# Performance work log

Hardware: AMD Instinct MI355X
Metric: run time of the kernel (lower is better)

## Reference

```python
import jax, jax.numpy as jnp
import numpy as np

SHRINK_THRES = 0.0025
EPS = 1e-12  # F.normalize default eps


def _l2norm(v, axis=-1):
    return v / jnp.maximum(jnp.linalg.norm(v, axis=axis, keepdims=True), EPS)


def setup_inputs() -> dict:
    key = jax.random.key(0)
    ks = jax.random.split(key, 5)
    N, C, H, W = 16, 256, 64, 64
    mem_dim = 512
    x = jax.random.normal(ks[0], (N, C, H, W), dtype=jnp.float32)
    memory = jax.random.normal(ks[1], (mem_dim, C), dtype=jnp.float32) * 0.1
    memory = _l2norm(memory, axis=1)
    w1 = jax.random.normal(ks[2], (C, C // 2), dtype=jnp.float32) * (1.0 / np.sqrt(C))
    b1 = jnp.zeros((C // 2,), dtype=jnp.float32)
    w2 = jax.random.normal(ks[3], (C // 2, C), dtype=jnp.float32) * (1.0 / np.sqrt(C // 2))
    b2 = jnp.zeros((C,), dtype=jnp.float32)
    return {"x": x, "memory": memory, "w1": w1, "b1": b1, "w2": w2, "b2": b2}


def reference(x, memory, w1, b1, w2, b2):
    N, C, H, W = x.shape
    # [N,C,H,W] -> [N*H*W, C]
    x_flat = jnp.transpose(x, (0, 2, 3, 1)).reshape(-1, C)
    x_norm = _l2norm(x_flat, axis=1)
    # shared MLP over memory slots: Linear -> ReLU -> Linear -> ReLU
    m = jax.nn.relu(memory @ w1 + b1)
    m = jax.nn.relu(m @ w2 + b2)
    mem_norm = _l2norm(m, axis=1)  # [M, C]
    # cosine similarity + softmax over memory slots
    att = jax.nn.softmax(x_norm @ mem_norm.T, axis=1)  # [N*H*W, M]
    # hard shrink + L1 renormalization
    att = jax.nn.relu(att - SHRINK_THRES)
    att = att / jnp.maximum(jnp.sum(att, axis=1, keepdims=True), EPS)
    out_flat = att @ mem_norm  # [N*H*W, C]
    output = jnp.transpose(out_flat.reshape(N, H, W, C), (0, 3, 1, 2))
    att_map = jnp.transpose(att.reshape(N, H, W, -1), (0, 3, 1, 2))
    return output, att_map
```

## Files before the change

### kernel.cpp

```cpp
#include <hip/hip_runtime.h>
#include <hip/hip_bf16.h>

typedef _Float16 half8 __attribute__((ext_vector_type(8)));
typedef _Float16 half4v __attribute__((ext_vector_type(4)));
typedef float floatx4 __attribute__((ext_vector_type(4)));

#define C_DIM 256
#define M_DIM 512
#define HW 4096
#define TAU 0.0025f
#define LCAP 96

__global__ __launch_bounds__(128) void prep_kernel(
    const float* __restrict__ memory, const float* __restrict__ w1,
    const float* __restrict__ b1, const float* __restrict__ w2,
    const float* __restrict__ b2,
    _Float16* __restrict__ mN, float* __restrict__ mN32,
    float* __restrict__ attmap)
{
  __shared__ float sm[256];
  __shared__ float sh[128];
  __shared__ float s_part[2];
  __shared__ float s_tot;
  const int r = blockIdx.x;
  const int t = threadIdx.x;

  {
    const floatx4 z = {0.f, 0.f, 0.f, 0.f};
    floatx4* p4 = (floatx4*)attmap;
    size_t i = (size_t)r * 128 + t;
#pragma unroll 4
    for (int k = 0; k < 128; ++k) { p4[i] = z; i += 65536; }
  }

  sm[t]       = memory[r * C_DIM + t];
  sm[t + 128] = memory[r * C_DIM + t + 128];
  __syncthreads();
  float acc = b1[t];
#pragma unroll 8
  for (int c = 0; c < 256; ++c) acc = fmaf(sm[c], w1[c * 128 + t], acc);
  sh[t] = fmaxf(acc, 0.f);
  __syncthreads();
  float o0 = b2[t], o1 = b2[t + 128];
#pragma unroll 8
  for (int k = 0; k < 128; ++k) {
    float h = sh[k];
    o0 = fmaf(h, w2[k * 256 + t], o0);
    o1 = fmaf(h, w2[k * 256 + t + 128], o1);
  }
  o0 = fmaxf(o0, 0.f);
  o1 = fmaxf(o1, 0.f);
  float ss = o0 * o0 + o1 * o1;
#pragma unroll
  for (int off = 32; off >= 1; off >>= 1) ss += __shfl_down(ss, off);
  if ((t & 63) == 0) s_part[t >> 6] = ss;
  __syncthreads();
  if (t == 0) s_tot = s_part[0] + s_part[1];
  __syncthreads();
  const float inv = 1.f / fmaxf(sqrtf(s_tot), 1e-12f);
  const float v0 = o0 * inv, v1 = o1 * inv;
  mN[r * C_DIM + t]        = (_Float16)v0;
  mN[r * C_DIM + t + 128]  = (_Float16)v1;
  mN32[r * C_DIM + t]       = v0;
  mN32[r * C_DIM + t + 128] = v1;
}

#define MFMA16(a, b, c) __builtin_amdgcn_mfma_f32_16x16x32_f16(a, b, c, 0, 0, 0)

__global__ __launch_bounds__(512, 4) void main_kernel(
    const float* __restrict__ x,
    const _Float16* __restrict__ mN,
    const float* __restrict__ mN32,
    float* __restrict__ out, float* __restrict__ attmap)
{
  __shared__ _Float16       Xh[64][264];
  __shared__ unsigned short s_lslot[64][LCAP];
  __shared__ float          s_lval[64][LCAP];
  __shared__ int      s_cnt[64];
  __shared__ float    s_sumsq[64];
  __shared__ float    s_sum1[64];
  __shared__ float    s_sum2[64];

  const int tid  = threadIdx.x;
  const int wave = tid >> 6;
  const int lane = tid & 63;
  const int q    = lane >> 4;
  const int c16  = lane & 15;
  const int g    = tid >> 3;
  const int pxq  = tid & 7;

  const int blk = blockIdx.x;
  const int img = blk >> 6;
  const int hw0 = (blk & 63) * 64;
  const float* __restrict__ xb = x + (size_t)img * C_DIM * HW + hw0;

  if (tid < 64) {
    s_sumsq[tid] = 0.f; s_sum1[tid] = 0.f; s_sum2[tid] = 0.f; s_cnt[tid] = 0;
  }
  __syncthreads();

#pragma unroll
  for (int h = 0; h < 2; ++h) {
    floatx4 v[4];
#pragma unroll
    for (int i = 0; i < 4; ++i)
      v[i] = *(const floatx4*)(xb + (size_t)(4 * g + i) * HW + (pxq + 8 * h) * 4);
    float ps[4];
#pragma unroll
    for (int j = 0; j < 4; ++j) {
      const int p = (pxq + 8 * h) * 4 + j;
      half4v hv = {(_Float16)v[0][j], (_Float16)v[1][j], (_Float16)v[2][j], (_Float16)v[3][j]};
      *(half4v*)&Xh[p][4 * g] = hv;
      ps[j] = v[0][j] * v[0][j] + v[1][j] * v[1][j] + v[2][j] * v[2][j] + v[3][j] * v[3][j];
    }
#pragma unroll
    for (int off = 8; off < 64; off <<= 1)
#pragma unroll
      for (int j = 0; j < 4; ++j) ps[j] += __shfl_xor(ps[j], off);
    if ((lane >> 3) == 0) {
#pragma unroll
      for (int j = 0; j < 4; ++j) atomicAdd(&s_sumsq[4 * (lane & 7) + 32 * h + j], ps[j]);
    }
  }

  const _Float16* bp[4];
#pragma unroll
  for (int nt = 0; nt < 4; ++nt)
    bp[nt] = mN + (size_t)(wave * 64 + nt * 16 + c16) * C_DIM + q * 8;
  half8 bcur[4], bnxt[4];
#pragma unroll
  for (int nt = 0; nt < 4; ++nt) bcur[nt] = *(const half8*)bp[nt];

  __syncthreads();

  floatx4 acc[4][4];
#pragma unroll
  for (int mt = 0; mt < 4; ++mt)
#pragma unroll
    for (int nt = 0; nt < 4; ++nt) {
      floatx4 z = {0.f, 0.f, 0.f, 0.f};
      acc[mt][nt] = z;
    }
#pragma unroll
  for (int kb = 0; kb < 8; ++kb) {
    if (kb < 7) {
#pragma unroll
      for (int nt = 0; nt < 4; ++nt) bnxt[nt] = *(const half8*)(bp[nt] + (kb + 1) * 32);
    }
    const int k0 = kb * 32 + q * 8;
    half8 ah[4];
#pragma unroll
    for (int mt = 0; mt < 4; ++mt) ah[mt] = *(const half8*)&Xh[mt * 16 + c16][k0];
#pragma unroll
    for (int nt = 0; nt < 4; ++nt)
#pragma unroll
      for (int mt = 0; mt < 4; ++mt)
        acc[mt][nt] = MFMA16(ah[mt], bcur[nt], acc[mt][nt]);
#pragma unroll
    for (int nt = 0; nt < 4; ++nt) bcur[nt] = bnxt[nt];
  }

#pragma unroll
  for (int mt = 0; mt < 4; ++mt)
#pragma unroll
    for (int r = 0; r < 4; ++r) {
      const int m = mt * 16 + q * 4 + r;
      const float iv = 1.f / fmaxf(sqrtf(s_sumsq[m]), 1e-12f);
      float s = 0.f;
#pragma unroll
      for (int nt = 0; nt < 4; ++nt) {
        const float e = __expf(acc[mt][nt][r] * iv);
        acc[mt][nt][r] = e;
        s += e;
      }
      s += __shfl_xor(s, 1);
      s += __shfl_xor(s, 2);
      s += __shfl_xor(s, 4);
      s += __shfl_xor(s, 8);
      if (c16 == 0) atomicAdd(&s_sum1[m], s);
    }
  __syncthreads();

#pragma unroll
  for (int mt = 0; mt < 4; ++mt)
#pragma unroll
    for (int r = 0; r < 4; ++r) {
      const int m = mt * 16 + q * 4 + r;
      const float isum = 1.f / s_sum1[m];
      float s = 0.f;
#pragma unroll
      for (int nt = 0; nt < 4; ++nt) {
        const float tv = fmaxf(acc[mt][nt][r] * isum - TAU, 0.f);
        acc[mt][nt][r] = tv;
        s += tv;
      }
      s += __shfl_xor(s, 1);
      s += __shfl_xor(s, 2);
      s += __shfl_xor(s, 4);
      s += __shfl_xor(s, 8);
      if (c16 == 0) atomicAdd(&s_sum2[m], s);
    }
  __syncthreads();

#pragma unroll
  for (int mt = 0; mt < 4; ++mt) {
    float rs[4];
#pragma unroll
    for (int r = 0; r < 4; ++r)
      rs[r] = 1.f / fmaxf(s_sum2[mt * 16 + q * 4 + r], 1e-12f);
#pragma unroll
    for (int nt = 0; nt < 4; ++nt) {
      floatx4 a4 = acc[mt][nt];
      const unsigned n = wave * 64 + nt * 16 + c16;
#pragma unroll
      for (int r = 0; r < 4; ++r) {
        a4[r] *= rs[r];
        if (a4[r] > 0.f) {
          const int m = mt * 16 + q * 4 + r;
          const int idx = atomicAdd(&s_cnt[m], 1);
          if (idx < LCAP) {
            s_lslot[m][idx] = (unsigned short)n;
            s_lval[m][idx]  = a4[r];
          }
          attmap[((size_t)img * M_DIM + n) * HW + hw0 + m] = a4[r];
        }
      }
    }
  }
  __syncthreads();

  const int px4 = (tid & 15) * 4;
  const int chg = tid >> 4;
  floatx4 f[8] = {{0.f,0.f,0.f,0.f},{0.f,0.f,0.f,0.f},{0.f,0.f,0.f,0.f},{0.f,0.f,0.f,0.f},
                  {0.f,0.f,0.f,0.f},{0.f,0.f,0.f,0.f},{0.f,0.f,0.f,0.f},{0.f,0.f,0.f,0.f}};
#pragma unroll
  for (int p = 0; p < 4; ++p) {
    const int cn = min(s_cnt[px4 + p], LCAP);
    for (int j = 0; j < cn; ++j) {
      const int slot  = s_lslot[px4 + p][j];
      const float v   = s_lval[px4 + p][j];
      const floatx4* row = (const floatx4*)(mN32 + (size_t)slot * C_DIM + chg * 8);
      const floatx4 r0 = row[0], r1 = row[1];
      f[0][p] += v * r0[0]; f[1][p] += v * r0[1];
      f[2][p] += v * r0[2]; f[3][p] += v * r0[3];
      f[4][p] += v * r1[0]; f[5][p] += v * r1[1];
      f[6][p] += v * r1[2]; f[7][p] += v * r1[3];
    }
  }

#pragma unroll
  for (int c = 0; c < 8; ++c)
    *(floatx4*)(out + ((size_t)img * C_DIM + chg * 8 + c) * HW + hw0 + px4) = f[c];
}

extern "C" void kernel_launch(void* const* d_in, const int* in_sizes, int n_in,
                              void* d_out, int out_size, void* d_ws, size_t ws_size,
                              hipStream_t stream) {
  (void)in_sizes; (void)n_in; (void)out_size; (void)ws_size;
  const float* x      = (const float*)d_in[0];
  const float* memory = (const float*)d_in[1];
  const float* w1     = (const float*)d_in[2];
  const float* b1     = (const float*)d_in[3];
  const float* w2     = (const float*)d_in[4];
  const float* b2     = (const float*)d_in[5];
  float* out    = (float*)d_out;
  float* attmap = out + (size_t)16 * C_DIM * HW;

  _Float16* mN   = (_Float16*)d_ws;
  float*    mN32 = (float*)((char*)d_ws + (size_t)M_DIM * C_DIM * sizeof(_Float16));

  hipLaunchKernelGGL(prep_kernel, dim3(M_DIM), dim3(128), 0, stream,
                     memory, w1, b1, w2, b2, mN, mN32, attmap);
  hipLaunchKernelGGL(main_kernel, dim3(1024), dim3(512), 0, stream,
                     x, mN, mN32, out, attmap);
}
```

Baseline: 323.5 us.

## Halve pixel tile, widen attmap zeroing grid, use nontemporal stores

The main kernel now processes 32 pixels per block instead of 64, doubling the grid to 2048 blocks and raising the occupancy hint to 6. The sparse slot list capacity drops from 96 to 16. The B-operand register double buffering is removed. The prep kernel runs 2048 blocks of 256 threads so the attmap zero-fill is spread wider, and it and the output writes use nontemporal stores. The aim is more parallelism and less LDS per block. LCAP=16 risks silently dropping nonzero attention entries when more than 16 slots survive the shrink threshold.

```diff
diff --git a/kernel.cpp b/kernel.cpp
--- a/kernel.cpp
+++ b/kernel.cpp
@@ -1,5 +1,4 @@
 #include <hip/hip_runtime.h>
-#include <hip/hip_bf16.h>
 
 typedef _Float16 half8 __attribute__((ext_vector_type(8)));
 typedef _Float16 half4v __attribute__((ext_vector_type(4)));
@@ -9,9 +8,9 @@
 #define M_DIM 512
 #define HW 4096
 #define TAU 0.0025f
-#define LCAP 96
-
-__global__ __launch_bounds__(128) void prep_kernel(
+#define LCAP 16
+
+__global__ __launch_bounds__(256) void prep_kernel(
     const float* __restrict__ memory, const float* __restrict__ w1,
     const float* __restrict__ b1, const float* __restrict__ w2,
     const float* __restrict__ b2,
@@ -27,59 +26,69 @@
 
   {
     const floatx4 z = {0.f, 0.f, 0.f, 0.f};
-    floatx4* p4 = (floatx4*)attmap;
-    size_t i = (size_t)r * 128 + t;
-#pragma unroll 4
-    for (int k = 0; k < 128; ++k) { p4[i] = z; i += 65536; }
-  }
-
-  sm[t]       = memory[r * C_DIM + t];
-  sm[t + 128] = memory[r * C_DIM + t + 128];
-  __syncthreads();
-  float acc = b1[t];
+    floatx4* p4 = (floatx4*)attmap + (size_t)r * 4096 + t;
+#pragma unroll
+    for (int k = 0; k < 16; ++k) __builtin_nontemporal_store(z, p4 + k * 256);
+  }
+  if (r >= M_DIM) return;
+
+  if (t < 128) {
+    sm[t]       = memory[r * C_DIM + t];
+    sm[t + 128] = memory[r * C_DIM + t + 128];
+  }
+  __syncthreads();
+  float o0 = 0.f, o1 = 0.f;
+  if (t < 128) {
+    float acc = b1[t];
 #pragma unroll 8
-  for (int c = 0; c < 256; ++c) acc = fmaf(sm[c], w1[c * 128 + t], acc);
-  sh[t] = fmaxf(acc, 0.f);
-  __syncthreads();
-  float o0 = b2[t], o1 = b2[t + 128];
+    for (int c = 0; c < 256; ++c) acc = fmaf(sm[c], w1[c * 128 + t], acc);
+    sh[t] = fmaxf(acc, 0.f);
+  }
+  __syncthreads();
+  if (t < 128) {
+    o0 = b2[t];
+    o1 = b2[t + 128];
 #pragma unroll 8
-  for (int k = 0; k < 128; ++k) {
-    float h = sh[k];
-    o0 = fmaf(h, w2[k * 256 + t], o0);
-    o1 = fmaf(h, w2[k * 256 + t + 128], o1);
-  }
-  o0 = fmaxf(o0, 0.f);
-  o1 = fmaxf(o1, 0.f);
-  float ss = o0 * o0 + o1 * o1;
-#pragma unroll
-  for (int off = 32; off >= 1; off >>= 1) ss += __shfl_down(ss, off);
-  if ((t & 63) == 0) s_part[t >> 6] = ss;
+    for (int k = 0; k < 128; ++k) {
+      float h = sh[k];
+      o0 = fmaf(h, w2[k * 256 + t], o0);
+      o1 = fmaf(h, w2[k * 256 + t + 128], o1);
+    }
+    o0 = fmaxf(o0, 0.f);
+    o1 = fmaxf(o1, 0.f);
+    float ss = o0 * o0 + o1 * o1;
+#pragma unroll
+    for (int off = 32; off >= 1; off >>= 1) ss += __shfl_down(ss, off);
+    if ((t & 63) == 0) s_part[t >> 6] = ss;
+  }
   __syncthreads();
   if (t == 0) s_tot = s_part[0] + s_part[1];
   __syncthreads();
-  const float inv = 1.f / fmaxf(sqrtf(s_tot), 1e-12f);
-  const float v0 = o0 * inv, v1 = o1 * inv;
-  mN[r * C_DIM + t]        = (_Float16)v0;
-  mN[r * C_DIM + t + 128]  = (_Float16)v1;
-  mN32[r * C_DIM + t]       = v0;
-  mN32[r * C_DIM + t + 128] = v1;
+  if (t < 128) {
+    const float inv = 1.f / fmaxf(sqrtf(s_tot), 1e-12f);
+    const float v0 = o0 * inv, v1 = o1 * inv;
+    mN[r * C_DIM + t]        = (_Float16)v0;
+    mN[r * C_DIM + t + 128]  = (_Float16)v1;
+    mN32[r * C_DIM + t]       = v0;
+    mN32[r * C_DIM + t + 128] = v1;
+  }
 }
 
 #define MFMA16(a, b, c) __builtin_amdgcn_mfma_f32_16x16x32_f16(a, b, c, 0, 0, 0)
 
-__global__ __launch_bounds__(512, 4) void main_kernel(
+__global__ __launch_bounds__(512, 6) void main_kernel(
     const float* __restrict__ x,
     const _Float16* __restrict__ mN,
     const float* __restrict__ mN32,
     float* __restrict__ out, float* __restrict__ attmap)
 {
-  __shared__ _Float16       Xh[64][264];
-  __shared__ unsigned short s_lslot[64][LCAP];
-  __shared__ float          s_lval[64][LCAP];
-  __shared__ int      s_cnt[64];
-  __shared__ float    s_sumsq[64];
-  __shared__ float    s_sum1[64];
-  __shared__ float    s_sum2[64];
+  __shared__ _Float16       Xh[32][264];
+  __shared__ unsigned short s_lslot[32][LCAP];
+  __shared__ float          s_lval[32][LCAP];
+  __shared__ int      s_cnt[32];
+  __shared__ float    s_sumsq[32];
+  __shared__ float    s_sum1[32];
+  __shared__ float    s_sum2[32];
 
   const int tid  = threadIdx.x;
   const int wave = tid >> 6;
@@ -90,25 +99,24 @@
   const int pxq  = tid & 7;
 
   const int blk = blockIdx.x;
-  const int img = blk >> 6;
-  const int hw0 = (blk & 63) * 64;
+  const int img = blk >> 7;
+  const int hw0 = (blk & 127) * 32;
   const float* __restrict__ xb = x + (size_t)img * C_DIM * HW + hw0;
 
-  if (tid < 64) {
+  if (tid < 32) {
     s_sumsq[tid] = 0.f; s_sum1[tid] = 0.f; s_sum2[tid] = 0.f; s_cnt[tid] = 0;
   }
   __syncthreads();
 
-#pragma unroll
-  for (int h = 0; h < 2; ++h) {
+  {
     floatx4 v[4];
 #pragma unroll
     for (int i = 0; i < 4; ++i)
-      v[i] = *(const floatx4*)(xb + (size_t)(4 * g + i) * HW + (pxq + 8 * h) * 4);
+      v[i] = *(const floatx4*)(xb + (size_t)(4 * g + i) * HW + pxq * 4);
     float ps[4];
 #pragma unroll
     for (int j = 0; j < 4; ++j) {
-      const int p = (pxq + 8 * h) * 4 + j;
+      const int p = pxq * 4 + j;
       half4v hv = {(_Float16)v[0][j], (_Float16)v[1][j], (_Float16)v[2][j], (_Float16)v[3][j]};
       *(half4v*)&Xh[p][4 * g] = hv;
       ps[j] = v[0][j] * v[0][j] + v[1][j] * v[1][j] + v[2][j] * v[2][j] + v[3][j] * v[3][j];
@@ -119,7 +127,7 @@
       for (int j = 0; j < 4; ++j) ps[j] += __shfl_xor(ps[j], off);
     if ((lane >> 3) == 0) {
 #pragma unroll
-      for (int j = 0; j < 4; ++j) atomicAdd(&s_sumsq[4 * (lane & 7) + 32 * h + j], ps[j]);
+      for (int j = 0; j < 4; ++j) atomicAdd(&s_sumsq[4 * (lane & 7) + j], ps[j]);
     }
   }
 
@@ -127,15 +135,12 @@
 #pragma unroll
   for (int nt = 0; nt < 4; ++nt)
     bp[nt] = mN + (size_t)(wave * 64 + nt * 16 + c16) * C_DIM + q * 8;
-  half8 bcur[4], bnxt[4];
-#pragma unroll
-  for (int nt = 0; nt < 4; ++nt) bcur[nt] = *(const half8*)bp[nt];
-
-  __syncthreads();
-
-  floatx4 acc[4][4];
-#pragma unroll
-  for (int mt = 0; mt < 4; ++mt)
+
+  __syncthreads();
+
+  floatx4 acc[2][4];
+#pragma unroll
+  for (int mt = 0; mt < 2; ++mt)
 #pragma unroll
     for (int nt = 0; nt < 4; ++nt) {
       floatx4 z = {0.f, 0.f, 0.f, 0.f};
@@ -143,25 +148,21 @@
     }
 #pragma unroll
   for (int kb = 0; kb < 8; ++kb) {
-    if (kb < 7) {
-#pragma unroll
-      for (int nt = 0; nt < 4; ++nt) bnxt[nt] = *(const half8*)(bp[nt] + (kb + 1) * 32);
-    }
+    half8 bv[4];
+#pragma unroll
+    for (int nt = 0; nt < 4; ++nt) bv[nt] = *(const half8*)(bp[nt] + kb * 32);
     const int k0 = kb * 32 + q * 8;
-    half8 ah[4];
-#pragma unroll
-    for (int mt = 0; mt < 4; ++mt) ah[mt] = *(const half8*)&Xh[mt * 16 + c16][k0];
-#pragma unroll
-    for (int nt = 0; nt < 4; ++nt)
-#pragma unroll
-      for (int mt = 0; mt < 4; ++mt)
-        acc[mt][nt] = MFMA16(ah[mt], bcur[nt], acc[mt][nt]);
-#pragma unroll
-    for (int nt = 0; nt < 4; ++nt) bcur[nt] = bnxt[nt];
-  }
-
-#pragma unroll
-  for (int mt = 0; mt < 4; ++mt)
+    half8 a0 = *(const half8*)&Xh[c16][k0];
+    half8 a1 = *(const half8*)&Xh[16 + c16][k0];
+#pragma unroll
+    for (int nt = 0; nt < 4; ++nt) {
+      acc[0][nt] = MFMA16(a0, bv[nt], acc[0][nt]);
+      acc[1][nt] = MFMA16(a1, bv[nt], acc[1][nt]);
+    }
+  }
+
+#pragma unroll
+  for (int mt = 0; mt < 2; ++mt)
 #pragma unroll
     for (int r = 0; r < 4; ++r) {
       const int m = mt * 16 + q * 4 + r;
@@ -182,7 +183,7 @@
   __syncthreads();
 
 #pragma unroll
-  for (int mt = 0; mt < 4; ++mt)
+  for (int mt = 0; mt < 2; ++mt)
 #pragma unroll
     for (int r = 0; r < 4; ++r) {
       const int m = mt * 16 + q * 4 + r;
@@ -203,7 +204,7 @@
   __syncthreads();
 
 #pragma unroll
-  for (int mt = 0; mt < 4; ++mt) {
+  for (int mt = 0; mt < 2; ++mt) {
     float rs[4];
 #pragma unroll
     for (int r = 0; r < 4; ++r)
@@ -229,28 +230,25 @@
   }
   __syncthreads();
 
-  const int px4 = (tid & 15) * 4;
-  const int chg = tid >> 4;
-  floatx4 f[8] = {{0.f,0.f,0.f,0.f},{0.f,0.f,0.f,0.f},{0.f,0.f,0.f,0.f},{0.f,0.f,0.f,0.f},
-                  {0.f,0.f,0.f,0.f},{0.f,0.f,0.f,0.f},{0.f,0.f,0.f,0.f},{0.f,0.f,0.f,0.f}};
+  const int px4 = (tid & 7) * 4;
+  const int chg = tid >> 3;
+  floatx4 f[4] = {{0.f,0.f,0.f,0.f},{0.f,0.f,0.f,0.f},{0.f,0.f,0.f,0.f},{0.f,0.f,0.f,0.f}};
 #pragma unroll
   for (int p = 0; p < 4; ++p) {
     const int cn = min(s_cnt[px4 + p], LCAP);
     for (int j = 0; j < cn; ++j) {
       const int slot  = s_lslot[px4 + p][j];
       const float v   = s_lval[px4 + p][j];
-      const floatx4* row = (const floatx4*)(mN32 + (size_t)slot * C_DIM + chg * 8);
-      const floatx4 r0 = row[0], r1 = row[1];
+      const floatx4 r0 = *(const floatx4*)(mN32 + (size_t)slot * C_DIM + chg * 4);
       f[0][p] += v * r0[0]; f[1][p] += v * r0[1];
       f[2][p] += v * r0[2]; f[3][p] += v * r0[3];
-      f[4][p] += v * r1[0]; f[5][p] += v * r1[1];
-      f[6][p] += v * r1[2]; f[7][p] += v * r1[3];
-    }
-  }
-
-#pragma unroll
-  for (int c = 0; c < 8; ++c)
-    *(floatx4*)(out + ((size_t)img * C_DIM + chg * 8 + c) * HW + hw0 + px4) = f[c];
+    }
+  }
+
+#pragma unroll
+  for (int c = 0; c < 4; ++c)
+    __builtin_nontemporal_store(
+        f[c], (floatx4*)(out + ((size_t)img * C_DIM + chg * 4 + c) * HW + hw0 + px4));
 }
 
 extern "C" void kernel_launch(void* const* d_in, const int* in_sizes, int n_in,
@@ -269,8 +267,8 @@
   _Float16* mN   = (_Float16*)d_ws;
   float*    mN32 = (float*)((char*)d_ws + (size_t)M_DIM * C_DIM * sizeof(_Float16));
 
-  hipLaunchKernelGGL(prep_kernel, dim3(M_DIM), dim3(128), 0, stream,
+  hipLaunchKernelGGL(prep_kernel, dim3(2048), dim3(256), 0, stream,
                      memory, w1, b1, w2, b2, mN, mN32, attmap);
-  hipLaunchKernelGGL(main_kernel, dim3(1024), dim3(512), 0, stream,
+  hipLaunchKernelGGL(main_kernel, dim3(2048), dim3(512), 0, stream,
                      x, mN, mN32, out, attmap);
 }
```

After: 345.6 us. +6.8%, slower.
